# Performance work log

Measured on AMD Instinct MI355X. Metric: run time of the kernel, lower is better.

Reference implementation:

```python
import jax, jax.numpy as jnp
import numpy as np

K = 3            # num_neighbors
C_IN = 128       # in_channels (== out_channels, required by fusion_kernel)
C_OUT = 128
B, H, W = 2, 64, 512
EPS = 1e-5       # BatchNorm eps (eval mode, running stats)


def _unfold(x, k):
    # F.unfold(x, k, padding=k//2).view(B, C, k*k, H*W); patch index = kh*k + kw
    b, c, h, w = x.shape
    p = k // 2
    xp = jnp.pad(x, ((0, 0), (0, 0), (p, p), (p, p)))
    patches = jnp.stack(
        [xp[:, :, i:i + h, j:j + w] for i in range(k) for j in range(k)], axis=2
    )  # (B, C, k*k, H, W)
    return patches.reshape(b, c, k * k, h * w)


def _conv1x1(x, w):
    # 1x1 Conv2d (bias=False) on (B, C, K^2, HW)
    return jnp.einsum('oc,bcnp->bonp', w, x)


def _bn(x, g, b, m, v):
    # BatchNorm2d in eval mode with running stats
    scale = (g / jnp.sqrt(v + EPS))[None, :, None, None]
    shift = (b - m * g / jnp.sqrt(v + EPS))[None, :, None, None]
    return x * scale + shift


def setup_inputs() -> dict:
    key = jax.random.key(0)
    ks = jax.random.split(key, 9)
    f32 = jnp.float32
    features = jax.random.normal(ks[0], (B, C_IN, H, W), f32)
    cart = jax.random.normal(ks[1], (B, 3, H, W), f32)
    mask = jax.random.bernoulli(ks[2], 0.9, (B, 1, H, W))

    def bn_params(k, c):
        k1, k2, k3, k4 = jax.random.split(k, 4)
        g = 1.0 + 0.1 * jax.random.normal(k1, (c,), f32)
        b = 0.1 * jax.random.normal(k2, (c,), f32)
        m = 0.1 * jax.random.normal(k3, (c,), f32)
        v = jax.random.uniform(k4, (c,), f32, 0.5, 1.5)
        return g, b, m, v

    pw = jax.random.normal(ks[3], (C_OUT, 3), f32) / jnp.sqrt(3.0)
    pg, pb, pm, pv = bn_params(ks[4], C_OUT)
    fw = jax.random.normal(ks[5], (C_OUT, C_IN), f32) / jnp.sqrt(float(C_IN))
    fg, fb, fm, fv = bn_params(ks[6], C_OUT)
    ew = jax.random.normal(ks[7], (3, C_OUT), f32) / jnp.sqrt(float(C_OUT))
    eg, eb, em, ev = bn_params(ks[8], 3)
    return dict(features=features, cart=cart, mask=mask,
                pw=pw, pg=pg, pb=pb, pm=pm, pv=pv,
                fw=fw, fg=fg, fb=fb, fm=fm, fv=fv,
                ew=ew, eg=eg, eb=eb, em=em, ev=ev)


def reference(features, cart, mask, pw, pg, pb, pm, pv,
              fw, fg, fb, fm, fv, ew, eg, eb, em, ev):
    b, c, h, w = features.shape
    fdt = features.dtype
    fe = _unfold(features, K)                      # (B, C, K^2, HW)
    cc = _unfold(cart, K)                          # (B, 3, K^2, HW)
    mu = _unfold(mask.astype(fdt), K)              # (B, 1, K^2, HW)
    center = (K * K) // 2
    rel = cc - cc[:, :, center:center + 1]         # relative coordinates
    pos = jax.nn.relu(_bn(_conv1x1(rel, pw), pg, pb, pm, pv))
    fe = jax.nn.relu(_bn(_conv1x1(fe, fw), fg, fb, fm, fv)) + pos
    geo = jnp.max(fe * mu, axis=2, keepdims=True)  # max_pool over K^2 neighbors
    e2c = _bn(_conv1x1(geo, ew), eg, eb, em, ev).reshape(b, 3, h, w)
    cart_out = cart + e2c * mask.astype(cart.dtype)
    return geo.reshape(b, -1, h, w), cart_out
```

## Files before the change

### kernel.cpp

```cpp
#include <hip/hip_runtime.h>

typedef unsigned short u16;
typedef unsigned int u32;
typedef unsigned char u8;

#define HW 32768
#define NPX 65536
#define GEO_SIZE 8388608
#define EPS 1e-5f

#define OFF_PWP   0
#define OFF_EWP   512
#define OFF_SHE   1024
#define OFF_FLG   1028
#define OFF_SHF   1088
#define W2T_OFF   8192
#define EAP_OFF   131072
#define T_OFF     8388608

#define LDS_STRIDE 136

typedef __bf16 bf16x8 __attribute__((ext_vector_type(8)));
typedef float f32x4 __attribute__((ext_vector_type(4)));

__device__ __forceinline__ float bf2f(u16 u){ return __uint_as_float(((u32)u) << 16); }
__device__ __forceinline__ u16 f2bf(float f){
  u32 x = __float_as_uint(f);
  return (u16)((x + 0x7fffu + ((x >> 16) & 1u)) >> 16);
}
__device__ __forceinline__ float bflo(u32 w){ return __uint_as_float(w << 16); }
__device__ __forceinline__ float bfhi(u32 w){ return __uint_as_float(w & 0xffff0000u); }

__device__ __forceinline__ float ldp(const void* p, int i, bool isbf){
  return isbf ? bf2f(((const u16*)p)[i]) : ((const float*)p)[i];
}

__device__ __forceinline__ bool sniff_bf16(const void* fv){
  const u16* w = (const u16*)fv;
  int hits = 0;
  for (int i = 0; i < 32; i++) {
    float v = bf2f(w[i]);
    hits += (v >= 0.45f && v <= 1.55f) ? 1 : 0;
  }
  return hits >= 26;
}

__device__ __forceinline__ int sniff_mask(const void* mask){
  const u8* mb = (const u8*)mask;
  int c01 = 0, ones = 0;
  for (int i = 0; i < 64; i++) { u8 v = mb[i]; c01 += (v <= 1); ones += (v == 1); }
  if (c01 == 64) return (ones >= 24) ? 0 : 1;
  const u16* mw = (const u16*)mask;
  int c3f = 0;
  for (int i = 0; i < 32; i++) c3f += (mw[i] == 0x3F80);
  return (c3f >= 22) ? 2 : 3;
}

__device__ __forceinline__ float mask_at(const void* m, int gi, int enc){
  if (enc == 0) return ((const u8*)m)[gi]  ? 1.f : 0.f;
  if (enc == 1) return ((const int*)m)[gi] ? 1.f : 0.f;
  if (enc == 2) return ((const u16*)m)[gi] ? 1.f : 0.f;
  return (((const float*)m)[gi] != 0.f) ? 1.f : 0.f;
}

__global__ void prep_kernel(const void* __restrict__ pw, const void* __restrict__ pg,
                            const void* __restrict__ pb, const void* __restrict__ pm,
                            const void* __restrict__ pv,
                            const void* __restrict__ fw, const void* __restrict__ fg,
                            const void* __restrict__ fb, const void* __restrict__ fm,
                            const void* __restrict__ fv,
                            const void* __restrict__ ew, const void* __restrict__ eg,
                            const void* __restrict__ eb, const void* __restrict__ em,
                            const void* __restrict__ ev,
                            const void* __restrict__ mask,
                            float* __restrict__ ws){
  int o = threadIdx.x;
  bool isbf = sniff_bf16(fv);
  if (o == 0) {
    ws[OFF_FLG]     = isbf ? 1.f : 0.f;
    ws[OFF_FLG + 1] = (float)sniff_mask(mask);
  }
  float sf = ldp(fg, o, isbf) / sqrtf(ldp(fv, o, isbf) + EPS);
  ws[OFF_SHF + o] = ldp(fb, o, isbf) - ldp(fm, o, isbf) * sf;
  u32* w2t = (u32*)((char*)ws + W2T_OFF);
  if (isbf) {
    const u32* fwp = (const u32*)fw;
    for (int c = 0; c < 128; c += 2) {
      u32 in = fwp[(o * 128 + c) >> 1];
      u32 lo = (u32)f2bf(sf * bf2f((u16)(in & 0xffff)));
      u32 hi = (u32)f2bf(sf * bf2f((u16)(in >> 16)));
      w2t[(o * 128 + c) >> 1] = lo | (hi << 16);
    }
  } else {
    const float* fwp = (const float*)fw;
    for (int c = 0; c < 128; c += 2) {
      u32 lo = (u32)f2bf(sf * fwp[o * 128 + c]);
      u32 hi = (u32)f2bf(sf * fwp[o * 128 + c + 1]);
      w2t[(o * 128 + c) >> 1] = lo | (hi << 16);
    }
  }
  float sp = ldp(pg, o, isbf) / sqrtf(ldp(pv, o, isbf) + EPS);
  float4* pwp = (float4*)(ws + OFF_PWP);
  pwp[o] = make_float4(sp * ldp(pw, o * 3 + 0, isbf),
                       sp * ldp(pw, o * 3 + 1, isbf),
                       sp * ldp(pw, o * 3 + 2, isbf),
                       ldp(pb, o, isbf) - ldp(pm, o, isbf) * sp);
  float se0 = ldp(eg, 0, isbf) / sqrtf(ldp(ev, 0, isbf) + EPS);
  float se1 = ldp(eg, 1, isbf) / sqrtf(ldp(ev, 1, isbf) + EPS);
  float se2 = ldp(eg, 2, isbf) / sqrtf(ldp(ev, 2, isbf) + EPS);
  float4* ewp = (float4*)(ws + OFF_EWP);
  ewp[o] = make_float4(se0 * ldp(ew, 0 * 128 + o, isbf),
                       se1 * ldp(ew, 1 * 128 + o, isbf),
                       se2 * ldp(ew, 2 * 128 + o, isbf), 0.f);
  if (o < 3) {
    float se = ldp(eg, o, isbf) / sqrtf(ldp(ev, o, isbf) + EPS);
    ws[OFF_SHE + o] = ldp(eb, o, isbf) - ldp(em, o, isbf) * se;
  }
}

__global__ __launch_bounds__(256) void stage1_kernel(const void* __restrict__ feat,
                                                     const float* __restrict__ ws,
                                                     u16* __restrict__ t){
  __shared__ u16 lds[128 * LDS_STRIDE];
  int tid = threadIdx.x;
  bool isbf = ws[OFF_FLG] > 0.5f;
  int pxg = blockIdx.x * 128;
  int b = pxg >> 15, hw0 = pxg & 32767;

  {
    int cp = tid & 63, q = tid >> 6;
    int c0 = cp * 2;
    long e0 = (long)(b * 128 + c0) * HW + hw0 + q * 32;
    u16* base = lds + (q * 32) * LDS_STRIDE + c0;
    if (isbf) {
      const uint4* g0 = (const uint4*)((const u16*)feat + e0);
      const uint4* g1 = (const uint4*)((const u16*)feat + e0 + HW);
#pragma unroll
      for (int i = 0; i < 4; i++) {
        uint4 a = g0[i], c = g1[i];
        u32 av[4] = {a.x, a.y, a.z, a.w};
        u32 cv[4] = {c.x, c.y, c.z, c.w};
#pragma unroll
        for (int k = 0; k < 4; k++) {
          u32 lo = (av[k] & 0xffffu) | (cv[k] << 16);
          u32 hi = (av[k] >> 16) | (cv[k] & 0xffff0000u);
          *(u32*)(base + (i * 8 + k * 2 + 0) * LDS_STRIDE) = lo;
          *(u32*)(base + (i * 8 + k * 2 + 1) * LDS_STRIDE) = hi;
        }
      }
    } else {
      const float4* g0 = (const float4*)((const float*)feat + e0);
      const float4* g1 = (const float4*)((const float*)feat + e0 + HW);
#pragma unroll
      for (int i = 0; i < 8; i++) {
        float4 a = g0[i], c = g1[i];
        float av[4] = {a.x, a.y, a.z, a.w};
        float cv[4] = {c.x, c.y, c.z, c.w};
#pragma unroll
        for (int k = 0; k < 4; k++) {
          u32 v = (u32)f2bf(av[k]) | ((u32)f2bf(cv[k]) << 16);
          *(u32*)(base + (i * 4 + k) * LDS_STRIDE) = v;
        }
      }
    }
  }
  __syncthreads();

  int wave = tid >> 6, lane = tid & 63;
  int ln = lane & 15, quad = lane >> 4;
  int pxw = wave * 32;
  const uint4* W = (const uint4*)((const char*)ws + W2T_OFF);

  f32x4 acc[8][2];
#pragma unroll
  for (int ot = 0; ot < 8; ot++)
#pragma unroll
    for (int pt = 0; pt < 2; pt++) acc[ot][pt] = (f32x4){0.f, 0.f, 0.f, 0.f};

#pragma unroll
  for (int ks = 0; ks < 4; ks++) {
    bf16x8 a[8], bfr[2];
#pragma unroll
    for (int ot = 0; ot < 8; ot++)
      a[ot] = __builtin_bit_cast(bf16x8, W[(ot * 16 + ln) * 16 + ks * 4 + quad]);
#pragma unroll
    for (int pt = 0; pt < 2; pt++)
      bfr[pt] = __builtin_bit_cast(bf16x8,
          *(const uint4*)(lds + (pxw + pt * 16 + ln) * LDS_STRIDE + ks * 32 + quad * 8));
#pragma unroll
    for (int ot = 0; ot < 8; ot++)
#pragma unroll
      for (int pt = 0; pt < 2; pt++)
        acc[ot][pt] = __builtin_amdgcn_mfma_f32_16x16x32_bf16(a[ot], bfr[pt], acc[ot][pt], 0, 0, 0);
  }
  __syncthreads();

  const float* shf = ws + OFF_SHF;
#pragma unroll
  for (int ot = 0; ot < 8; ot++) {
#pragma unroll
    for (int r = 0; r < 4; r++) {
      int o = ot * 16 + quad * 4 + r;
      float s = shf[o];
#pragma unroll
      for (int pt = 0; pt < 2; pt++) {
        float v = fmaxf(acc[ot][pt][r] + s, 0.f);
        lds[o * LDS_STRIDE + pxw + pt * 16 + ln] = f2bf(v);
      }
    }
  }
  __syncthreads();
  {
    int o = tid >> 1, half = tid & 1;
    const u16* src = lds + o * LDS_STRIDE + half * 64;
    uint4* dst = (uint4*)(t + o * NPX + pxg + half * 64);
#pragma unroll
    for (int k = 0; k < 8; k++) dst[k] = *(const uint4*)(src + k * 8);
  }
}

__global__ __launch_bounds__(256) void stage2_kernel(const void* __restrict__ cart,
                                                     const float* __restrict__ ws,
                                                     const void* __restrict__ rawmask,
                                                     const u16* __restrict__ t,
                                                     float* __restrict__ eap,
                                                     void* __restrict__ out){
  int tid = threadIdx.x;
  int pxb = blockIdx.x & 127, grp = blockIdx.x >> 7;
  int px0 = pxb * 512 + tid * 2;
  int b = px0 >> 15, hw = px0 & 32767;
  int h = hw >> 9, w = hw & 511;
  bool isbf = ws[OFF_FLG] > 0.5f;
  int enc = (int)ws[OFF_FLG + 1];

  float rel[2][9][3];
  float mvv[12];
  {
    float cr[12][3];
#pragma unroll
    for (int r = 0; r < 3; r++) {
#pragma unroll
      for (int c = 0; c < 4; c++) {
        int idx = r * 4 + c;
        int h2 = h + r - 1, w2 = w + c - 1;
        bool ok = ((unsigned)h2 < 64u) && ((unsigned)w2 < 512u);
        int hw2 = ok ? ((h2 << 9) | w2) : hw;
        int gi = b * HW + hw2;
        float mval = mask_at(rawmask, gi, enc);
        mvv[idx] = ok ? mval : 0.f;
#pragma unroll
        for (int d = 0; d < 3; d++)
          cr[idx][d] = isbf ? bf2f(((const u16*)cart)[(b * 3 + d) * HW + hw2])
                            : ((const float*)cart)[(b * 3 + d) * HW + hw2];
      }
    }
#pragma unroll
    for (int r = 0; r < 3; r++)
#pragma unroll
      for (int cc = 0; cc < 3; cc++)
#pragma unroll
        for (int d = 0; d < 3; d++) {
          rel[0][r * 3 + cc][d] = cr[r * 4 + cc][d]     - cr[5][d];
          rel[1][r * 3 + cc][d] = cr[r * 4 + cc + 1][d] - cr[6][d];
        }
  }

  const float4* pwp = (const float4*)(ws + OFF_PWP);
  const float4* ewp = (const float4*)(ws + OFF_EWP);
  float ea00 = 0.f, ea01 = 0.f, ea02 = 0.f;
  float ea10 = 0.f, ea11 = 0.f, ea12 = 0.f;
  u16* o16 = (u16*)out;
  float* of = (float*)out;

#pragma unroll 4
  for (int j = 0; j < 16; j++) {
    int o = grp * 16 + j;
    const u16* tb = t + o * NPX + b * HW;
    u32 tw[3][3];
#pragma unroll
    for (int r = 0; r < 3; r++) {
      const u32* rp = (const u32*)(tb + (h + r - 1) * 512 + (w - 2));
      tw[r][0] = rp[0]; tw[r][1] = rp[1]; tw[r][2] = rp[2];
    }
    float4 P = pwp[o];
    float g0 = 0.f, g1 = 0.f;
#pragma unroll
    for (int r = 0; r < 3; r++) {
      float tm1 = bfhi(tw[r][0]);
      float t0  = bflo(tw[r][1]);
      float tp1 = bfhi(tw[r][1]);
      float tp2 = bflo(tw[r][2]);
      float tv0[3] = {tm1, t0, tp1};
      float tv1[3] = {t0, tp1, tp2};
#pragma unroll
      for (int cc = 0; cc < 3; cc++) {
        int n = r * 3 + cc;
        float pos0 = fmaxf(fmaf(P.x, rel[0][n][0],
                           fmaf(P.y, rel[0][n][1],
                           fmaf(P.z, rel[0][n][2], P.w))), 0.f);
        g0 = fmaxf(g0, (tv0[cc] + pos0) * mvv[r * 4 + cc]);
        float pos1 = fmaxf(fmaf(P.x, rel[1][n][0],
                           fmaf(P.y, rel[1][n][1],
                           fmaf(P.z, rel[1][n][2], P.w))), 0.f);
        g1 = fmaxf(g1, (tv1[cc] + pos1) * mvv[r * 4 + cc + 1]);
      }
    }
    int gi = (b * 128 + o) * HW + hw;
    if (isbf) *(u32*)(o16 + gi) = (u32)f2bf(g0) | ((u32)f2bf(g1) << 16);
    else { of[gi] = g0; of[gi + 1] = g1; }
    float4 E = ewp[o];
    ea00 = fmaf(E.x, g0, ea00); ea01 = fmaf(E.y, g0, ea01); ea02 = fmaf(E.z, g0, ea02);
    ea10 = fmaf(E.x, g1, ea10); ea11 = fmaf(E.y, g1, ea11); ea12 = fmaf(E.z, g1, ea12);
  }
  float2* ep;
  ep = (float2*)(eap + (grp * 3 + 0) * NPX + px0); *ep = make_float2(ea00, ea10);
  ep = (float2*)(eap + (grp * 3 + 1) * NPX + px0); *ep = make_float2(ea01, ea11);
  ep = (float2*)(eap + (grp * 3 + 2) * NPX + px0); *ep = make_float2(ea02, ea12);
}

__global__ __launch_bounds__(256) void final_kernel(const void* __restrict__ cart,
                                                    const float* __restrict__ ws,
                                                    const void* __restrict__ rawmask,
                                                    const float* __restrict__ eap,
                                                    void* __restrict__ out){
  int px0 = (blockIdx.x * 256 + threadIdx.x) * 2;
  int b = px0 >> 15, hw = px0 & 32767;
  bool isbf = ws[OFF_FLG] > 0.5f;
  int enc = (int)ws[OFF_FLG + 1];
  float s0a = 0.f, s0b = 0.f, s1a = 0.f, s1b = 0.f, s2a = 0.f, s2b = 0.f;
#pragma unroll
  for (int g = 0; g < 8; g++) {
    float2 v0 = *(const float2*)(eap + (g * 3 + 0) * NPX + px0);
    float2 v1 = *(const float2*)(eap + (g * 3 + 1) * NPX + px0);
    float2 v2 = *(const float2*)(eap + (g * 3 + 2) * NPX + px0);
    s0a += v0.x; s0b += v0.y;
    s1a += v1.x; s1b += v1.y;
    s2a += v2.x; s2b += v2.y;
  }
  float m0 = mask_at(rawmask, b * HW + hw, enc);
  float m1 = mask_at(rawmask, b * HW + hw + 1, enc);
  float she0 = ws[OFF_SHE], she1 = ws[OFF_SHE + 1], she2 = ws[OFF_SHE + 2];
  float c0a, c0b, c1a, c1b, c2a, c2b;
  if (isbf) {
    const u16* cb = (const u16*)cart + b * 3 * HW;
    c0a = bf2f(cb[hw]); c0b = bf2f(cb[hw + 1]);
    c1a = bf2f(cb[HW + hw]); c1b = bf2f(cb[HW + hw + 1]);
    c2a = bf2f(cb[2 * HW + hw]); c2b = bf2f(cb[2 * HW + hw + 1]);
  } else {
    const float* cb = (const float*)cart + b * 3 * HW;
    c0a = cb[hw]; c0b = cb[hw + 1];
    c1a = cb[HW + hw]; c1b = cb[HW + hw + 1];
    c2a = cb[2 * HW + hw]; c2b = cb[2 * HW + hw + 1];
  }
  float r0a = c0a + (s0a + she0) * m0, r0b = c0b + (s0b + she0) * m1;
  float r1a = c1a + (s1a + she1) * m0, r1b = c1b + (s1b + she1) * m1;
  float r2a = c2a + (s2a + she2) * m0, r2b = c2b + (s2b + she2) * m1;
  int cbase = GEO_SIZE + b * 3 * HW + hw;
  if (isbf) {
    u16* o16 = (u16*)out;
    *(u32*)(o16 + cbase)          = (u32)f2bf(r0a) | ((u32)f2bf(r0b) << 16);
    *(u32*)(o16 + cbase + HW)     = (u32)f2bf(r1a) | ((u32)f2bf(r1b) << 16);
    *(u32*)(o16 + cbase + 2 * HW) = (u32)f2bf(r2a) | ((u32)f2bf(r2b) << 16);
  } else {
    float* of = (float*)out;
    of[cbase] = r0a; of[cbase + 1] = r0b;
    of[cbase + HW] = r1a; of[cbase + HW + 1] = r1b;
    of[cbase + 2 * HW] = r2a; of[cbase + 2 * HW + 1] = r2b;
  }
}

extern "C" void kernel_launch(void* const* d_in, const int* in_sizes, int n_in,
                              void* d_out, int out_size, void* d_ws, size_t ws_size,
                              hipStream_t stream) {
  const void* feat = d_in[0];
  const void* cart = d_in[1];
  const void* mask = d_in[2];
  float* ws  = (float*)d_ws;
  float* eap = (float*)((char*)d_ws + EAP_OFF);
  u16*  t    = (u16*)((char*)d_ws + T_OFF);

  hipLaunchKernelGGL(prep_kernel, dim3(1), dim3(128), 0, stream,
                     d_in[3], d_in[4], d_in[5], d_in[6], d_in[7],
                     d_in[8], d_in[9], d_in[10], d_in[11], d_in[12],
                     d_in[13], d_in[14], d_in[15], d_in[16], d_in[17],
                     mask, ws);
  hipLaunchKernelGGL(stage1_kernel, dim3(512), dim3(256), 0, stream, feat, ws, t);
  hipLaunchKernelGGL(stage2_kernel, dim3(1024), dim3(256), 0, stream, cart, ws, mask, t, eap, d_out);
  hipLaunchKernelGGL(final_kernel, dim3(128), dim3(256), 0, stream, cart, ws, mask, eap, d_out);
}
```

Baseline: 169.0 us.

## Parallelize weight prep, pack stage2 math into float2 ops, halve channel groups

```diff
diff --git a/kernel.cpp b/kernel.cpp
--- a/kernel.cpp
+++ b/kernel.cpp
@@ -22,6 +22,7 @@
 
 typedef __bf16 bf16x8 __attribute__((ext_vector_type(8)));
 typedef float f32x4 __attribute__((ext_vector_type(4)));
+typedef float f32x2 __attribute__((ext_vector_type(2)));
 
 __device__ __forceinline__ float bf2f(u16 u){ return __uint_as_float(((u32)u) << 16); }
 __device__ __forceinline__ u16 f2bf(float f){
@@ -30,6 +31,13 @@
 }
 __device__ __forceinline__ float bflo(u32 w){ return __uint_as_float(w << 16); }
 __device__ __forceinline__ float bfhi(u32 w){ return __uint_as_float(w & 0xffff0000u); }
+
+__device__ __forceinline__ f32x2 pk_fma(f32x2 a, f32x2 b, f32x2 c){
+  return __builtin_elementwise_fma(a, b, c);
+}
+__device__ __forceinline__ f32x2 pk_max(f32x2 a, f32x2 b){
+  return __builtin_elementwise_max(a, b);
+}
 
 __device__ __forceinline__ float ldp(const void* p, int i, bool isbf){
   return isbf ? bf2f(((const u16*)p)[i]) : ((const float*)p)[i];
@@ -63,58 +71,61 @@
   return (((const float*)m)[gi] != 0.f) ? 1.f : 0.f;
 }
 
-__global__ void prep_kernel(const void* __restrict__ pw, const void* __restrict__ pg,
-                            const void* __restrict__ pb, const void* __restrict__ pm,
-                            const void* __restrict__ pv,
-                            const void* __restrict__ fw, const void* __restrict__ fg,
-                            const void* __restrict__ fb, const void* __restrict__ fm,
-                            const void* __restrict__ fv,
-                            const void* __restrict__ ew, const void* __restrict__ eg,
-                            const void* __restrict__ eb, const void* __restrict__ em,
-                            const void* __restrict__ ev,
-                            const void* __restrict__ mask,
-                            float* __restrict__ ws){
-  int o = threadIdx.x;
+__global__ __launch_bounds__(256) void prep_kernel(
+    const void* __restrict__ pw, const void* __restrict__ pg,
+    const void* __restrict__ pb, const void* __restrict__ pm,
+    const void* __restrict__ pv,
+    const void* __restrict__ fw, const void* __restrict__ fg,
+    const void* __restrict__ fb, const void* __restrict__ fm,
+    const void* __restrict__ fv,
+    const void* __restrict__ ew, const void* __restrict__ eg,
+    const void* __restrict__ eb, const void* __restrict__ em,
+    const void* __restrict__ ev,
+    const void* __restrict__ mask,
+    float* __restrict__ ws){
+  int blk = blockIdx.x, tid = threadIdx.x;
   bool isbf = sniff_bf16(fv);
+  if (blk < 32) {
+    int p = blk * 256 + tid;
+    int o = p >> 6;
+    float sf = ldp(fg, o, isbf) * __frsqrt_rn(ldp(fv, o, isbf) + EPS);
+    u32 outv;
+    if (isbf) {
+      u32 in = ((const u32*)fw)[p];
+      outv = (u32)f2bf(sf * bf2f((u16)(in & 0xffff))) |
+             ((u32)f2bf(sf * bf2f((u16)(in >> 16))) << 16);
+    } else {
+      const float* fwp = (const float*)fw;
+      outv = (u32)f2bf(sf * fwp[2 * p]) | ((u32)f2bf(sf * fwp[2 * p + 1]) << 16);
+    }
+    ((u32*)((char*)ws + W2T_OFF))[p] = outv;
+    return;
+  }
+  int o = tid;
   if (o == 0) {
     ws[OFF_FLG]     = isbf ? 1.f : 0.f;
     ws[OFF_FLG + 1] = (float)sniff_mask(mask);
   }
-  float sf = ldp(fg, o, isbf) / sqrtf(ldp(fv, o, isbf) + EPS);
-  ws[OFF_SHF + o] = ldp(fb, o, isbf) - ldp(fm, o, isbf) * sf;
-  u32* w2t = (u32*)((char*)ws + W2T_OFF);
-  if (isbf) {
-    const u32* fwp = (const u32*)fw;
-    for (int c = 0; c < 128; c += 2) {
-      u32 in = fwp[(o * 128 + c) >> 1];
-      u32 lo = (u32)f2bf(sf * bf2f((u16)(in & 0xffff)));
-      u32 hi = (u32)f2bf(sf * bf2f((u16)(in >> 16)));
-      w2t[(o * 128 + c) >> 1] = lo | (hi << 16);
-    }
-  } else {
-    const float* fwp = (const float*)fw;
-    for (int c = 0; c < 128; c += 2) {
-      u32 lo = (u32)f2bf(sf * fwp[o * 128 + c]);
-      u32 hi = (u32)f2bf(sf * fwp[o * 128 + c + 1]);
-      w2t[(o * 128 + c) >> 1] = lo | (hi << 16);
-    }
-  }
-  float sp = ldp(pg, o, isbf) / sqrtf(ldp(pv, o, isbf) + EPS);
-  float4* pwp = (float4*)(ws + OFF_PWP);
-  pwp[o] = make_float4(sp * ldp(pw, o * 3 + 0, isbf),
-                       sp * ldp(pw, o * 3 + 1, isbf),
-                       sp * ldp(pw, o * 3 + 2, isbf),
-                       ldp(pb, o, isbf) - ldp(pm, o, isbf) * sp);
-  float se0 = ldp(eg, 0, isbf) / sqrtf(ldp(ev, 0, isbf) + EPS);
-  float se1 = ldp(eg, 1, isbf) / sqrtf(ldp(ev, 1, isbf) + EPS);
-  float se2 = ldp(eg, 2, isbf) / sqrtf(ldp(ev, 2, isbf) + EPS);
-  float4* ewp = (float4*)(ws + OFF_EWP);
-  ewp[o] = make_float4(se0 * ldp(ew, 0 * 128 + o, isbf),
-                       se1 * ldp(ew, 1 * 128 + o, isbf),
-                       se2 * ldp(ew, 2 * 128 + o, isbf), 0.f);
-  if (o < 3) {
-    float se = ldp(eg, o, isbf) / sqrtf(ldp(ev, o, isbf) + EPS);
-    ws[OFF_SHE + o] = ldp(eb, o, isbf) - ldp(em, o, isbf) * se;
+  if (o < 128) {
+    float sf = ldp(fg, o, isbf) * __frsqrt_rn(ldp(fv, o, isbf) + EPS);
+    ws[OFF_SHF + o] = ldp(fb, o, isbf) - ldp(fm, o, isbf) * sf;
+    float sp = ldp(pg, o, isbf) * __frsqrt_rn(ldp(pv, o, isbf) + EPS);
+    float4* pwp = (float4*)(ws + OFF_PWP);
+    pwp[o] = make_float4(sp * ldp(pw, o * 3 + 0, isbf),
+                         sp * ldp(pw, o * 3 + 1, isbf),
+                         sp * ldp(pw, o * 3 + 2, isbf),
+                         ldp(pb, o, isbf) - ldp(pm, o, isbf) * sp);
+    float se0 = ldp(eg, 0, isbf) * __frsqrt_rn(ldp(ev, 0, isbf) + EPS);
+    float se1 = ldp(eg, 1, isbf) * __frsqrt_rn(ldp(ev, 1, isbf) + EPS);
+    float se2 = ldp(eg, 2, isbf) * __frsqrt_rn(ldp(ev, 2, isbf) + EPS);
+    float4* ewp = (float4*)(ws + OFF_EWP);
+    ewp[o] = make_float4(se0 * ldp(ew, 0 * 128 + o, isbf),
+                         se1 * ldp(ew, 1 * 128 + o, isbf),
+                         se2 * ldp(ew, 2 * 128 + o, isbf), 0.f);
+    if (o < 3) {
+      float se = ldp(eg, o, isbf) * __frsqrt_rn(ldp(ev, o, isbf) + EPS);
+      ws[OFF_SHE + o] = ldp(eb, o, isbf) - ldp(em, o, isbf) * se;
+    }
   }
 }
 
@@ -233,10 +244,11 @@
   bool isbf = ws[OFF_FLG] > 0.5f;
   int enc = (int)ws[OFF_FLG + 1];
 
-  float rel[2][9][3];
-  float mvv[12];
+  f32x2 rel2[9][3];
+  f32x2 mv2[9];
   {
     float cr[12][3];
+    float mm[12];
 #pragma unroll
     for (int r = 0; r < 3; r++) {
 #pragma unroll
@@ -246,8 +258,7 @@
         bool ok = ((unsigned)h2 < 64u) && ((unsigned)w2 < 512u);
         int hw2 = ok ? ((h2 << 9) | w2) : hw;
         int gi = b * HW + hw2;
-        float mval = mask_at(rawmask, gi, enc);
-        mvv[idx] = ok ? mval : 0.f;
+        mm[idx] = ok ? mask_at(rawmask, gi, enc) : 0.f;
 #pragma unroll
         for (int d = 0; d < 3; d++)
           cr[idx][d] = isbf ? bf2f(((const u16*)cart)[(b * 3 + d) * HW + hw2])
@@ -257,24 +268,26 @@
 #pragma unroll
     for (int r = 0; r < 3; r++)
 #pragma unroll
-      for (int cc = 0; cc < 3; cc++)
-#pragma unroll
-        for (int d = 0; d < 3; d++) {
-          rel[0][r * 3 + cc][d] = cr[r * 4 + cc][d]     - cr[5][d];
-          rel[1][r * 3 + cc][d] = cr[r * 4 + cc + 1][d] - cr[6][d];
-        }
+      for (int cc = 0; cc < 3; cc++) {
+        int n = r * 3 + cc;
+        mv2[n] = (f32x2){mm[r * 4 + cc], mm[r * 4 + cc + 1]};
+#pragma unroll
+        for (int d = 0; d < 3; d++)
+          rel2[n][d] = (f32x2){cr[r * 4 + cc][d] - cr[5][d],
+                               cr[r * 4 + cc + 1][d] - cr[6][d]};
+      }
   }
 
   const float4* pwp = (const float4*)(ws + OFF_PWP);
   const float4* ewp = (const float4*)(ws + OFF_EWP);
-  float ea00 = 0.f, ea01 = 0.f, ea02 = 0.f;
-  float ea10 = 0.f, ea11 = 0.f, ea12 = 0.f;
+  f32x2 eA = {0.f, 0.f}, eB = {0.f, 0.f}, eC = {0.f, 0.f};
   u16* o16 = (u16*)out;
   float* of = (float*)out;
+  const f32x2 zero2 = {0.f, 0.f};
 
 #pragma unroll 4
-  for (int j = 0; j < 16; j++) {
-    int o = grp * 16 + j;
+  for (int j = 0; j < 32; j++) {
+    int o = grp * 32 + j;
     const u16* tb = t + o * NPX + b * HW;
     u32 tw[3][3];
 #pragma unroll
@@ -283,39 +296,35 @@
       tw[r][0] = rp[0]; tw[r][1] = rp[1]; tw[r][2] = rp[2];
     }
     float4 P = pwp[o];
-    float g0 = 0.f, g1 = 0.f;
+    f32x2 Px = {P.x, P.x}, Py = {P.y, P.y}, Pz = {P.z, P.z}, Pw = {P.w, P.w};
+    f32x2 g = {0.f, 0.f};
 #pragma unroll
     for (int r = 0; r < 3; r++) {
       float tm1 = bfhi(tw[r][0]);
       float t0  = bflo(tw[r][1]);
       float tp1 = bfhi(tw[r][1]);
       float tp2 = bflo(tw[r][2]);
-      float tv0[3] = {tm1, t0, tp1};
-      float tv1[3] = {t0, tp1, tp2};
+      f32x2 tv[3] = {{tm1, t0}, {t0, tp1}, {tp1, tp2}};
 #pragma unroll
       for (int cc = 0; cc < 3; cc++) {
         int n = r * 3 + cc;
-        float pos0 = fmaxf(fmaf(P.x, rel[0][n][0],
-                           fmaf(P.y, rel[0][n][1],
-                           fmaf(P.z, rel[0][n][2], P.w))), 0.f);
-        g0 = fmaxf(g0, (tv0[cc] + pos0) * mvv[r * 4 + cc]);
-        float pos1 = fmaxf(fmaf(P.x, rel[1][n][0],
-                           fmaf(P.y, rel[1][n][1],
-                           fmaf(P.z, rel[1][n][2], P.w))), 0.f);
-        g1 = fmaxf(g1, (tv1[cc] + pos1) * mvv[r * 4 + cc + 1]);
+        f32x2 pos = pk_max(pk_fma(Px, rel2[n][0],
+                           pk_fma(Py, rel2[n][1],
+                           pk_fma(Pz, rel2[n][2], Pw))), zero2);
+        g = pk_max(g, (tv[cc] + pos) * mv2[n]);
       }
     }
     int gi = (b * 128 + o) * HW + hw;
-    if (isbf) *(u32*)(o16 + gi) = (u32)f2bf(g0) | ((u32)f2bf(g1) << 16);
-    else { of[gi] = g0; of[gi + 1] = g1; }
+    if (isbf) *(u32*)(o16 + gi) = (u32)f2bf(g.x) | ((u32)f2bf(g.y) << 16);
+    else { of[gi] = g.x; of[gi + 1] = g.y; }
     float4 E = ewp[o];
-    ea00 = fmaf(E.x, g0, ea00); ea01 = fmaf(E.y, g0, ea01); ea02 = fmaf(E.z, g0, ea02);
-    ea10 = fmaf(E.x, g1, ea10); ea11 = fmaf(E.y, g1, ea11); ea12 = fmaf(E.z, g1, ea12);
-  }
-  float2* ep;
-  ep = (float2*)(eap + (grp * 3 + 0) * NPX + px0); *ep = make_float2(ea00, ea10);
-  ep = (float2*)(eap + (grp * 3 + 1) * NPX + px0); *ep = make_float2(ea01, ea11);
-  ep = (float2*)(eap + (grp * 3 + 2) * NPX + px0); *ep = make_float2(ea02, ea12);
+    eA = pk_fma((f32x2){E.x, E.x}, g, eA);
+    eB = pk_fma((f32x2){E.y, E.y}, g, eB);
+    eC = pk_fma((f32x2){E.z, E.z}, g, eC);
+  }
+  *(f32x2*)(eap + (grp * 3 + 0) * NPX + px0) = eA;
+  *(f32x2*)(eap + (grp * 3 + 1) * NPX + px0) = eB;
+  *(f32x2*)(eap + (grp * 3 + 2) * NPX + px0) = eC;
 }
 
 __global__ __launch_bounds__(256) void final_kernel(const void* __restrict__ cart,
@@ -327,15 +336,12 @@
   int b = px0 >> 15, hw = px0 & 32767;
   bool isbf = ws[OFF_FLG] > 0.5f;
   int enc = (int)ws[OFF_FLG + 1];
-  float s0a = 0.f, s0b = 0.f, s1a = 0.f, s1b = 0.f, s2a = 0.f, s2b = 0.f;
-#pragma unroll
-  for (int g = 0; g < 8; g++) {
-    float2 v0 = *(const float2*)(eap + (g * 3 + 0) * NPX + px0);
-    float2 v1 = *(const float2*)(eap + (g * 3 + 1) * NPX + px0);
-    float2 v2 = *(const float2*)(eap + (g * 3 + 2) * NPX + px0);
-    s0a += v0.x; s0b += v0.y;
-    s1a += v1.x; s1b += v1.y;
-    s2a += v2.x; s2b += v2.y;
+  f32x2 s0 = {0.f, 0.f}, s1 = {0.f, 0.f}, s2 = {0.f, 0.f};
+#pragma unroll
+  for (int g = 0; g < 4; g++) {
+    s0 += *(const f32x2*)(eap + (g * 3 + 0) * NPX + px0);
+    s1 += *(const f32x2*)(eap + (g * 3 + 1) * NPX + px0);
+    s2 += *(const f32x2*)(eap + (g * 3 + 2) * NPX + px0);
   }
   float m0 = mask_at(rawmask, b * HW + hw, enc);
   float m1 = mask_at(rawmask, b * HW + hw + 1, enc);
@@ -352,9 +358,9 @@
     c1a = cb[HW + hw]; c1b = cb[HW + hw + 1];
     c2a = cb[2 * HW + hw]; c2b = cb[2 * HW + hw + 1];
   }
-  float r0a = c0a + (s0a + she0) * m0, r0b = c0b + (s0b + she0) * m1;
-  float r1a = c1a + (s1a + she1) * m0, r1b = c1b + (s1b + she1) * m1;
-  float r2a = c2a + (s2a + she2) * m0, r2b = c2b + (s2b + she2) * m1;
+  float r0a = c0a + (s0.x + she0) * m0, r0b = c0b + (s0.y + she0) * m1;
+  float r1a = c1a + (s1.x + she1) * m0, r1b = c1b + (s1.y + she1) * m1;
+  float r2a = c2a + (s2.x + she2) * m0, r2b = c2b + (s2.y + she2) * m1;
   int cbase = GEO_SIZE + b * 3 * HW + hw;
   if (isbf) {
     u16* o16 = (u16*)out;
@@ -379,12 +385,12 @@
   float* eap = (float*)((char*)d_ws + EAP_OFF);
   u16*  t    = (u16*)((char*)d_ws + T_OFF);
 
-  hipLaunchKernelGGL(prep_kernel, dim3(1), dim3(128), 0, stream,
+  hipLaunchKernelGGL(prep_kernel, dim3(33), dim3(256), 0, stream,
                      d_in[3], d_in[4], d_in[5], d_in[6], d_in[7],
                      d_in[8], d_in[9], d_in[10], d_in[11], d_in[12],
                      d_in[13], d_in[14], d_in[15], d_in[16], d_in[17],
                      mask, ws);
   hipLaunchKernelGGL(stage1_kernel, dim3(512), dim3(256), 0, stream, feat, ws, t);
-  hipLaunchKernelGGL(stage2_kernel, dim3(1024), dim3(256), 0, stream, cart, ws, mask, t, eap, d_out);
+  hipLaunchKernelGGL(stage2_kernel, dim3(512), dim3(256), 0, stream, cart, ws, mask, t, eap, d_out);
   hipLaunchKernelGGL(final_kernel, dim3(128), dim3(256), 0, stream, cart, ws, mask, eap, d_out);
 }
```

After: 164.9 us. 1.02x faster.
